# Optimization experiments

Hardware: AMD Instinct MI355X
Metric: run time of the kernel (lower is better)

The kernel has to match this reference:

```python
import jax, jax.numpy as jnp
import numpy as np

B, C, D, W, H = 8, 256, 24, 24, 24
COUT = 256
EMBED = 128
HEADS = 8
WORD = 64
POOL = 3  # forward hardcodes adaptive_avg_pool3d(x, 3)


def setup_inputs() -> dict:
    key = jax.random.key(0)
    ks = jax.random.split(key, 12)
    s = lambda n: 1.0 / np.sqrt(n)
    return {
        "x": jax.random.normal(ks[0], (B, C, D, W, H), dtype=jnp.float32),
        "qk_w": jax.random.normal(ks[1], (2 * EMBED, POOL ** 3), dtype=jnp.float32) * s(POOL ** 3),
        "qk_b": jax.random.normal(ks[2], (2 * EMBED,), dtype=jnp.float32) * 0.02,
        "wq_w": jax.random.normal(ks[3], (HEADS * WORD, EMBED), dtype=jnp.float32) * s(EMBED),
        "wq_b": jax.random.normal(ks[4], (HEADS * WORD,), dtype=jnp.float32) * 0.02,
        "wk_w": jax.random.normal(ks[5], (HEADS * WORD, EMBED), dtype=jnp.float32) * s(EMBED),
        "wk_b": jax.random.normal(ks[6], (HEADS * WORD,), dtype=jnp.float32) * 0.02,
        "fch_w": jax.random.normal(ks[7], (1, HEADS), dtype=jnp.float32) * s(HEADS),
        "fch_b": jax.random.normal(ks[8], (1,), dtype=jnp.float32) * 0.02,
        "conv_w": jax.random.normal(ks[9], (COUT, C), dtype=jnp.float32) * s(C),
        "conv_b": jax.random.normal(ks[10], (COUT,), dtype=jnp.float32) * 0.02,
    }


def reference(x, qk_w, qk_b, wq_w, wq_b, wk_w, wk_b, fch_w, fch_b, conv_w, conv_b):
    b, c, d, w, h = x.shape
    # adaptive_avg_pool3d to 3x3x3 (exact: dims divisible by 3) -> [b, c, 27]
    xmean = x.reshape(b, c, POOL, d // POOL, POOL, w // POOL, POOL, h // POOL)
    xmean = xmean.mean(axis=(3, 5, 7)).reshape(b, c, POOL ** 3)
    # qk projection -> split into q, k of [b, c, embed]
    qk = xmean @ qk_w.T + qk_b                      # [b, c, 2*embed]
    qk = qk.reshape(b, c, 2, EMBED)
    q, k = qk[:, :, 0], qk[:, :, 1]
    # head projections -> [b, heads, c, word]
    q = (q @ wq_w.T + wq_b).reshape(b, c, HEADS, WORD).transpose(0, 2, 1, 3)
    k = (k @ wk_w.T + wk_b).reshape(b, c, HEADS, WORD).transpose(0, 2, 1, 3)
    # channel attention: scores over channels [b, heads, c, c]
    scores = jnp.einsum("bhcw,bhkw->bhck", q / jnp.sqrt(jnp.float32(WORD)), k)
    attn = jax.nn.softmax(scores, axis=-1)          # dropout is identity in eval
    # v is the raw spatial map [b, c, d*w*h]; broadcast over heads
    v = x.reshape(b, c, d * w * h)
    y = jnp.einsum("bhck,bkn->bhcn", attn, v)       # [b, heads, c, dwh]
    # fch: Linear(heads, 1) combining heads
    y = jnp.einsum("bhcn,h->bcn", y, fch_w[0]) + fch_b[0]
    y = y.reshape(b, c, d, w, h)
    attn_out = jnp.einsum("bhck,h->bck", attn, fch_w[0]) + fch_b[0]  # [b, c, c]
    # 1x1x1 conv residual
    out = jnp.einsum("bcxyz,oc->boxyz", y + x, conv_w) + conv_b[None, :, None, None, None]
    return (out, attn_out)
```

## Files before the change

kernel.cpp:

```cpp
#include <hip/hip_runtime.h>
#include <cstdint>
#include <cstddef>

#define B_    8
#define C_    256
#define DWH   13824
#define P3    27
#define COUT_ 256

#define OFF_XMEAN 0
#define OFF_WQT   55296
#define OFF_WKT   69120
#define OFF_BQ    82944
#define OFF_BK    83456
#define OFF_BETA  83968
#define OFF_G     84224
#define OFF_U     90272
#define OFF_V     90488
#define OFF_D     90704
#define OFF_ZT    90712
#define OFF_A     549464
#define OFF_MHI   1073752
#define OFF_MLO   1335896

typedef __attribute__((ext_vector_type(8))) short bf16x8;
typedef __attribute__((ext_vector_type(4))) float f32x4;

__device__ __forceinline__ void split_bf16(float v, unsigned short& h, unsigned short& l) {
    unsigned u  = __float_as_uint(v);
    unsigned hu = u & 0xFFFF0000u;
    float r = v - __uint_as_float(hu);
    h = (unsigned short)(u >> 16);
    l = (unsigned short)(__float_as_uint(r) >> 16);
}

__global__ __launch_bounds__(256) void k_pool(const float* __restrict__ x,
                                              float* __restrict__ xmean) {
    int bc = blockIdx.x;
    __shared__ float p0[576], p1[576], p2[576];
    const float* xb = x + (size_t)bc * DWH;
    for (int t = threadIdx.x; t < 576; t += 256) {
        int g  = t >> 6;
        int s  = t & 63;
        int pd = g / 3, pw = g % 3;
        int d  = pd * 8 + (s >> 3);
        int w  = pw * 8 + (s & 7);
        const float4* r = (const float4*)(xb + ((size_t)d * 24 + w) * 24);
        float4 f0 = r[0], f1 = r[1], f2 = r[2], f3 = r[3], f4v = r[4], f5 = r[5];
        p0[t] = f0.x + f0.y + f0.z + f0.w + f1.x + f1.y + f1.z + f1.w;
        p1[t] = f2.x + f2.y + f2.z + f2.w + f3.x + f3.y + f3.z + f3.w;
        p2[t] = f4v.x + f4v.y + f4v.z + f4v.w + f5.x + f5.y + f5.z + f5.w;
    }
    __syncthreads();
    int tid = threadIdx.x;
    if (tid < 27) {
        int pd = tid / 9, pw = (tid / 3) % 3, ph = tid % 3;
        int g = pd * 3 + pw;
        const float* src = (ph == 0) ? p0 : (ph == 1 ? p1 : p2);
        float s = 0.f;
        #pragma unroll 8
        for (int i = 0; i < 64; ++i) s += src[g * 64 + i];
        xmean[(size_t)bc * P3 + tid] = s * (1.0f / 512.0f);
    }
}

__global__ __launch_bounds__(128) void k_combine(
    const float* __restrict__ qk_w, const float* __restrict__ qk_b,
    const float* __restrict__ wq_w, const float* __restrict__ wq_b,
    const float* __restrict__ wk_w, const float* __restrict__ wk_b,
    const float* __restrict__ fch_b, const float* __restrict__ conv_w,
    const float* __restrict__ conv_b,
    float* __restrict__ WqT, float* __restrict__ WkT,
    float* __restrict__ bq, float* __restrict__ bk, float* __restrict__ beta) {
    int t = blockIdx.x * 128 + threadIdx.x;
    if (t < 13824) {
        int j = t / 27, p = t % 27;
        float s = 0.f;
        for (int e = 0; e < 128; ++e) s += wq_w[j * 128 + e] * qk_w[e * 27 + p];
        WqT[p * 512 + j] = s;
    } else if (t < 27648) {
        int u = t - 13824, j = u / 27, p = u % 27;
        float s = 0.f;
        for (int e = 0; e < 128; ++e) s += wk_w[j * 128 + e] * qk_w[(128 + e) * 27 + p];
        WkT[p * 512 + j] = s;
    } else if (t < 28160) {
        int j = t - 27648;
        float s = wq_b[j];
        for (int e = 0; e < 128; ++e) s += wq_w[j * 128 + e] * qk_b[e];
        bq[j] = s;
    } else if (t < 28672) {
        int j = t - 28160;
        float s = wk_b[j];
        for (int e = 0; e < 128; ++e) s += wk_w[j * 128 + e] * qk_b[128 + e];
        bk[j] = s;
    } else if (t < 28928) {
        int o = t - 28672;
        float s = 0.f;
        for (int c = 0; c < 256; ++c) s += conv_w[o * 256 + c];
        beta[o] = fch_b[0] * s + conv_b[o];
    }
}

__global__ __launch_bounds__(256) void k_G(
    const float* __restrict__ WqT, const float* __restrict__ WkT,
    const float* __restrict__ bq, const float* __restrict__ bk,
    float* __restrict__ G, float* __restrict__ U,
    float* __restrict__ V, float* __restrict__ D) {
    int h = blockIdx.x;
    int base = h * 64;
    for (int idx = threadIdx.x; idx < 811; idx += 256) {
        if (idx < 756) {
            int p = idx / 28, r = idx % 28;
            float s = 0.f;
            if (r < 27)
                for (int w = 0; w < 64; ++w)
                    s += WqT[p * 512 + base + w] * WkT[r * 512 + base + w];
            G[(h * 27 + p) * 28 + r] = 0.125f * s;
        } else if (idx < 783) {
            int p = idx - 756;
            float s = 0.f;
            for (int w = 0; w < 64; ++w) s += WqT[p * 512 + base + w] * bk[base + w];
            V[h * 27 + p] = 0.125f * s;
        } else if (idx < 810) {
            int r = idx - 783;
            float s = 0.f;
            for (int w = 0; w < 64; ++w) s += WkT[r * 512 + base + w] * bq[base + w];
            U[h * 27 + r] = 0.125f * s;
        } else {
            float s = 0.f;
            for (int w = 0; w < 64; ++w) s += bq[base + w] * bk[base + w];
            D[h] = 0.125f * s;
        }
    }
}

__global__ __launch_bounds__(256) void k_z(
    const float* __restrict__ xmean, const float* __restrict__ G,
    const float* __restrict__ U, const float* __restrict__ V,
    const float* __restrict__ D, float* __restrict__ ZT) {
    int h = blockIdx.x, b = blockIdx.y;
    int k = threadIdx.x;
    __shared__ float Gs[756], Us[27], Vs[27], Ds;
    for (int idx = threadIdx.x; idx < 756; idx += 256) Gs[idx] = G[h * 756 + idx];
    if (threadIdx.x < 27) { Us[threadIdx.x] = U[h * 27 + threadIdx.x];
                            Vs[threadIdx.x] = V[h * 27 + threadIdx.x]; }
    if (threadIdx.x == 27) Ds = D[h];
    __syncthreads();
    float xm[28];
    const float* xp = xmean + ((size_t)(b * C_) + k) * P3;
    #pragma unroll
    for (int r = 0; r < 27; ++r) xm[r] = xp[r];
    xm[27] = 0.f;
    float z[28];
    #pragma unroll
    for (int p = 0; p < 27; ++p) {
        float acc = Vs[p];
        #pragma unroll
        for (int r4 = 0; r4 < 7; ++r4) {
            float4 g = *(const float4*)&Gs[p * 28 + r4 * 4];
            acc += g.x * xm[r4 * 4] + g.y * xm[r4 * 4 + 1]
                 + g.z * xm[r4 * 4 + 2] + g.w * xm[r4 * 4 + 3];
        }
        z[p] = acc;
    }
    {
        float e = Ds;
        #pragma unroll
        for (int r = 0; r < 27; ++r) e += Us[r] * xm[r];
        z[27] = e;
    }
    float4* zt = (float4*)ZT;
    int bh = b * 8 + h;
    #pragma unroll
    for (int p4 = 0; p4 < 7; ++p4) {
        float4 v = {z[p4 * 4], z[p4 * 4 + 1], z[p4 * 4 + 2], z[p4 * 4 + 3]};
        zt[((size_t)(bh * 7 + p4)) * 256 + k] = v;
    }
}

__global__ __launch_bounds__(256) void k_attn(
    const float* __restrict__ xmean, const float* __restrict__ ZT,
    const float* __restrict__ fch_w, const float* __restrict__ fch_b,
    float* __restrict__ A, float* __restrict__ attn_out) {
    int b = blockIdx.y;
    int c0 = blockIdx.x * 4;
    int t = threadIdx.x;
    int lane = t & 63, wv = t >> 6;
    __shared__ float xsh[4 * 28];
    __shared__ float ss[4][256];
    __shared__ float mx[4], den[4];
    if (t < 112) {
        int i = t / 28, p = t % 28;
        xsh[t] = (p < 27) ? xmean[((size_t)(b * C_) + c0 + i) * P3 + p] : 1.0f;
    }
    __syncthreads();
    float4 xr[4][7];
    #pragma unroll
    for (int cl = 0; cl < 4; ++cl)
        #pragma unroll
        for (int p4 = 0; p4 < 7; ++p4)
            xr[cl][p4] = *(const float4*)&xsh[cl * 28 + p4 * 4];
    float areg[4] = {0.f, 0.f, 0.f, 0.f};
    const float4* zt = (const float4*)ZT;
    for (int h = 0; h < 8; ++h) {
        int bh = b * 8 + h;
        float4 zk[7];
        #pragma unroll
        for (int p4 = 0; p4 < 7; ++p4)
            zk[p4] = zt[((size_t)(bh * 7 + p4)) * 256 + t];
        #pragma unroll
        for (int cl = 0; cl < 4; ++cl) {
            float dot = 0.f;
            #pragma unroll
            for (int p4 = 0; p4 < 7; ++p4) {
                float4 xv = xr[cl][p4];
                float4 zv = zk[p4];
                dot += xv.x * zv.x + xv.y * zv.y + xv.z * zv.z + xv.w * zv.w;
            }
            ss[cl][t] = dot;
        }
        __syncthreads();
        {
            int cl = wv;
            float4 v = *(const float4*)&ss[cl][lane * 4];
            float m = fmaxf(fmaxf(v.x, v.y), fmaxf(v.z, v.w));
            for (int off = 32; off; off >>= 1) m = fmaxf(m, __shfl_xor(m, off, 64));
            float s = expf(v.x - m) + expf(v.y - m) + expf(v.z - m) + expf(v.w - m);
            for (int off = 32; off; off >>= 1) s += __shfl_xor(s, off, 64);
            if (lane == 0) { mx[cl] = m; den[cl] = s; }
        }
        __syncthreads();
        float fw = fch_w[h];
        #pragma unroll
        for (int cl = 0; cl < 4; ++cl)
            areg[cl] += expf(ss[cl][t] - mx[cl]) * (fw / den[cl]);
        __syncthreads();
    }
    float fb = fch_b[0];
    #pragma unroll
    for (int cl = 0; cl < 4; ++cl) {
        size_t idx = ((size_t)(b * C_) + c0 + cl) * C_ + t;
        A[idx] = areg[cl];
        attn_out[idx] = areg[cl] + fb;
    }
}

__global__ __launch_bounds__(256) void k_M(
    const float* __restrict__ A, const float* __restrict__ conv_w,
    unsigned short* __restrict__ Mhi, unsigned short* __restrict__ Mlo) {
    int b = blockIdx.y;
    int o0 = blockIdx.x * 8;
    int t = threadIdx.x;
    __shared__ float cw[8][256];
    #pragma unroll
    for (int r = 0; r < 8; ++r) cw[r][t] = conv_w[(o0 + r) * 256 + t];
    __syncthreads();
    float acc[8] = {0.f, 0.f, 0.f, 0.f, 0.f, 0.f, 0.f, 0.f};
    const float* Ab = A + (size_t)b * C_ * C_;
    for (int c = 0; c < 256; ++c) {
        float av = Ab[(size_t)c * 256 + t];
        #pragma unroll
        for (int r = 0; r < 8; ++r) acc[r] += cw[r][c] * av;
    }
    #pragma unroll
    for (int r = 0; r < 8; ++r) {
        float mv = acc[r] + conv_w[(o0 + r) * 256 + t];
        unsigned short h, l;
        split_bf16(mv, h, l);
        size_t idx = ((size_t)(b * C_) + o0 + r) * 256 + t;
        Mhi[idx] = h;
        Mlo[idx] = l;
    }
}

__global__ __launch_bounds__(256, 2) void k_out_mfma(
    const unsigned short* __restrict__ Mhi, const unsigned short* __restrict__ Mlo,
    const float* __restrict__ x, const float* __restrict__ beta,
    float* __restrict__ out) {
    int b  = blockIdx.y;
    int n0 = blockIdx.x * 64;
    int t  = threadIdx.x;
    int lane = t & 63, wv = t >> 6;
    int wo   = wv * 64;
    int l15  = lane & 15;
    int kseg = lane >> 4;
    int kbyte = kseg * 16;

    __shared__ __align__(16) unsigned short MsH[256 * 32];
    __shared__ __align__(16) unsigned short MsL[256 * 32];
    __shared__ __align__(16) unsigned short XsH[64 * 32];
    __shared__ __align__(16) unsigned short XsL[64 * 32];

    f32x4 acc[4][4];
    #pragma unroll
    for (int m = 0; m < 4; ++m)
        #pragma unroll
        for (int nf = 0; nf < 4; ++nf) acc[m][nf] = (f32x4){0.f, 0.f, 0.f, 0.f};

    const float* xb = x + (size_t)b * 256 * DWH;
    const unsigned short* gh = Mhi + (size_t)b * 256 * 256;
    const unsigned short* gl = Mlo + (size_t)b * 256 * 256;

    for (int k0 = 0; k0 < 256; k0 += 32) {
        if (k0) __syncthreads();
        {
            int c4   = t & 3;
            int orow = t >> 2;
            #pragma unroll
            for (int it = 0; it < 4; ++it) {
                int o = it * 64 + orow;
                size_t gidx = (size_t)o * 256 + k0 + c4 * 8;
                uint4 vh = *(const uint4*)(gh + gidx);
                uint4 vl = *(const uint4*)(gl + gidx);
                int off = o * 64 + ((c4 * 16) ^ ((o & 3) << 4));
                *(uint4*)((char*)MsH + off) = vh;
                *(uint4*)((char*)MsL + off) = vl;
            }
        }
        {
            int n     = t & 63;
            int khalf = t >> 6;
            const float* xcol = xb + (size_t)(k0 + khalf * 8) * DWH + n0 + n;
            unsigned h[8], l[8];
            #pragma unroll
            for (int j = 0; j < 8; ++j) {
                float v = xcol[(size_t)j * DWH];
                unsigned short hh, ll;
                split_bf16(v, hh, ll);
                h[j] = hh; l[j] = ll;
            }
            uint4 vh, vl;
            vh.x = h[0] | (h[1] << 16); vh.y = h[2] | (h[3] << 16);
            vh.z = h[4] | (h[5] << 16); vh.w = h[6] | (h[7] << 16);
            vl.x = l[0] | (l[1] << 16); vl.y = l[2] | (l[3] << 16);
            vl.z = l[4] | (l[5] << 16); vl.w = l[6] | (l[7] << 16);
            int off = n * 64 + ((khalf * 16) ^ ((n & 3) << 4));
            *(uint4*)((char*)XsH + off) = vh;
            *(uint4*)((char*)XsL + off) = vl;
        }
        __syncthreads();
        bf16x8 Ah[4], Al[4], Bh[4], Bl[4];
        #pragma unroll
        for (int m = 0; m < 4; ++m) {
            int o = wo + m * 16 + l15;
            int off = o * 64 + (kbyte ^ ((o & 3) << 4));
            Ah[m] = *(const bf16x8*)((const char*)MsH + off);
            Al[m] = *(const bf16x8*)((const char*)MsL + off);
        }
        #pragma unroll
        for (int nf = 0; nf < 4; ++nf) {
            int n = nf * 16 + l15;
            int off = n * 64 + (kbyte ^ ((n & 3) << 4));
            Bh[nf] = *(const bf16x8*)((const char*)XsH + off);
            Bl[nf] = *(const bf16x8*)((const char*)XsL + off);
        }
        #pragma unroll
        for (int m = 0; m < 4; ++m)
            #pragma unroll
            for (int nf = 0; nf < 4; ++nf) {
                f32x4 c = acc[m][nf];
                c = __builtin_amdgcn_mfma_f32_16x16x32_bf16(Al[m], Bh[nf], c, 0, 0, 0);
                c = __builtin_amdgcn_mfma_f32_16x16x32_bf16(Ah[m], Bl[nf], c, 0, 0, 0);
                c = __builtin_amdgcn_mfma_f32_16x16x32_bf16(Ah[m], Bh[nf], c, 0, 0, 0);
                acc[m][nf] = c;
            }
    }

    int r4 = (lane >> 4) * 4;
    #pragma unroll
    for (int m = 0; m < 4; ++m) {
        int obase = wo + m * 16 + r4;
        float bet[4];
        #pragma unroll
        for (int r = 0; r < 4; ++r) bet[r] = beta[obase + r];
        #pragma unroll
        for (int nf = 0; nf < 4; ++nf) {
            int n = n0 + nf * 16 + l15;
            #pragma unroll
            for (int r = 0; r < 4; ++r)
                out[((size_t)(b * 256 + obase + r)) * DWH + n] = acc[m][nf][r] + bet[r];
        }
    }
}

extern "C" void kernel_launch(void* const* d_in, const int* in_sizes, int n_in,
                              void* d_out, int out_size, void* d_ws, size_t ws_size,
                              hipStream_t stream) {
    const float* x      = (const float*)d_in[0];
    const float* qk_w   = (const float*)d_in[1];
    const float* qk_b   = (const float*)d_in[2];
    const float* wq_w   = (const float*)d_in[3];
    const float* wq_b   = (const float*)d_in[4];
    const float* wk_w   = (const float*)d_in[5];
    const float* wk_b   = (const float*)d_in[6];
    const float* fch_w  = (const float*)d_in[7];
    const float* fch_b  = (const float*)d_in[8];
    const float* conv_w = (const float*)d_in[9];
    const float* conv_b = (const float*)d_in[10];
    float* out = (float*)d_out;
    float* attn_out = out + (size_t)B_ * COUT_ * DWH;
    float* ws = (float*)d_ws;
    unsigned short* Mhi = (unsigned short*)(ws + OFF_MHI);
    unsigned short* Mlo = (unsigned short*)(ws + OFF_MLO);

    k_pool<<<B_ * C_, 256, 0, stream>>>(x, ws + OFF_XMEAN);
    k_combine<<<226, 128, 0, stream>>>(qk_w, qk_b, wq_w, wq_b, wk_w, wk_b,
                                       fch_b, conv_w, conv_b,
                                       ws + OFF_WQT, ws + OFF_WKT,
                                       ws + OFF_BQ, ws + OFF_BK, ws + OFF_BETA);
    k_G<<<8, 256, 0, stream>>>(ws + OFF_WQT, ws + OFF_WKT, ws + OFF_BQ, ws + OFF_BK,
                               ws + OFF_G, ws + OFF_U, ws + OFF_V, ws + OFF_D);
    k_z<<<dim3(8, B_), 256, 0, stream>>>(ws + OFF_XMEAN, ws + OFF_G, ws + OFF_U,
                                         ws + OFF_V, ws + OFF_D, ws + OFF_ZT);
    k_attn<<<dim3(64, B_), 256, 0, stream>>>(ws + OFF_XMEAN, ws + OFF_ZT, fch_w, fch_b,
                                             ws + OFF_A, attn_out);
    k_M<<<dim3(32, B_), 256, 0, stream>>>(ws + OFF_A, conv_w, Mhi, Mlo);
    k_out_mfma<<<dim3(216, B_), 256, 0, stream>>>(Mhi, Mlo, x, ws + OFF_BETA, out);
}
```

Baseline: 145.0 us.

## Fuse prep kernels, pre-pack M fragments, and cut MFMA passes on x

```diff
diff --git a/kernel.cpp b/kernel.cpp
--- a/kernel.cpp
+++ b/kernel.cpp
@@ -9,19 +9,11 @@
 #define COUT_ 256
 
 #define OFF_XMEAN 0
-#define OFF_WQT   55296
-#define OFF_WKT   69120
-#define OFF_BQ    82944
-#define OFF_BK    83456
-#define OFF_BETA  83968
-#define OFF_G     84224
-#define OFF_U     90272
-#define OFF_V     90488
-#define OFF_D     90704
-#define OFF_ZT    90712
-#define OFF_A     549464
-#define OFF_MHI   1073752
-#define OFF_MLO   1335896
+#define OFF_BETA  55296
+#define OFF_ZT    55552
+#define OFF_A     514304
+#define OFF_MPH   1038592
+#define OFF_MPL   1300736
 
 typedef __attribute__((ext_vector_type(8))) short bf16x8;
 typedef __attribute__((ext_vector_type(4))) float f32x4;
@@ -32,6 +24,13 @@
     float r = v - __uint_as_float(hu);
     h = (unsigned short)(u >> 16);
     l = (unsigned short)(__float_as_uint(r) >> 16);
+}
+
+__device__ __forceinline__ unsigned rne2(float a, float b) {
+    unsigned ua = __float_as_uint(a), ub = __float_as_uint(b);
+    unsigned ra = (ua + 0x7FFFu + ((ua >> 16) & 1u)) >> 16;
+    unsigned rb = (ub + 0x7FFFu + ((ub >> 16) & 1u)) >> 16;
+    return ra | (rb << 16);
 }
 
 __global__ __launch_bounds__(256) void k_pool(const float* __restrict__ x,
@@ -64,88 +63,63 @@
     }
 }
 
-__global__ __launch_bounds__(128) void k_combine(
+__global__ __launch_bounds__(256) void k_prep(
     const float* __restrict__ qk_w, const float* __restrict__ qk_b,
     const float* __restrict__ wq_w, const float* __restrict__ wq_b,
     const float* __restrict__ wk_w, const float* __restrict__ wk_b,
-    const float* __restrict__ fch_b, const float* __restrict__ conv_w,
-    const float* __restrict__ conv_b,
-    float* __restrict__ WqT, float* __restrict__ WkT,
-    float* __restrict__ bq, float* __restrict__ bk, float* __restrict__ beta) {
-    int t = blockIdx.x * 128 + threadIdx.x;
-    if (t < 13824) {
-        int j = t / 27, p = t % 27;
-        float s = 0.f;
-        for (int e = 0; e < 128; ++e) s += wq_w[j * 128 + e] * qk_w[e * 27 + p];
-        WqT[p * 512 + j] = s;
-    } else if (t < 27648) {
-        int u = t - 13824, j = u / 27, p = u % 27;
-        float s = 0.f;
-        for (int e = 0; e < 128; ++e) s += wk_w[j * 128 + e] * qk_w[(128 + e) * 27 + p];
-        WkT[p * 512 + j] = s;
-    } else if (t < 28160) {
-        int j = t - 27648;
-        float s = wq_b[j];
-        for (int e = 0; e < 128; ++e) s += wq_w[j * 128 + e] * qk_b[e];
-        bq[j] = s;
-    } else if (t < 28672) {
-        int j = t - 28160;
-        float s = wk_b[j];
-        for (int e = 0; e < 128; ++e) s += wk_w[j * 128 + e] * qk_b[128 + e];
-        bk[j] = s;
-    } else if (t < 28928) {
-        int o = t - 28672;
-        float s = 0.f;
-        for (int c = 0; c < 256; ++c) s += conv_w[o * 256 + c];
-        beta[o] = fch_b[0] * s + conv_b[o];
-    }
-}
-
-__global__ __launch_bounds__(256) void k_G(
-    const float* __restrict__ WqT, const float* __restrict__ WkT,
-    const float* __restrict__ bq, const float* __restrict__ bk,
-    float* __restrict__ G, float* __restrict__ U,
-    float* __restrict__ V, float* __restrict__ D) {
-    int h = blockIdx.x;
-    int base = h * 64;
-    for (int idx = threadIdx.x; idx < 811; idx += 256) {
+    const float* __restrict__ xmean, float* __restrict__ ZT) {
+    int h = blockIdx.x, b = blockIdx.y;
+    int t = threadIdx.x;
+    __shared__ float Wq[P3][64], Wk[P3][64];
+    __shared__ float bqs[64], bks[64];
+    __shared__ float Gs[756], Us[P3], Vs[P3], Ds;
+    for (int idx = t; idx < 1728; idx += 256) {
+        int p = idx >> 6, w = idx & 63;
+        int row = h * 64 + w;
+        float sq = 0.f, sk = 0.f;
+        for (int e = 0; e < 128; ++e) {
+            float wqv = wq_w[row * 128 + e];
+            float wkv = wk_w[row * 128 + e];
+            sq += wqv * qk_w[e * 27 + p];
+            sk += wkv * qk_w[(128 + e) * 27 + p];
+        }
+        Wq[p][w] = sq; Wk[p][w] = sk;
+    }
+    if (t < 64) {
+        int row = h * 64 + t;
+        float s1 = wq_b[row], s2 = wk_b[row];
+        for (int e = 0; e < 128; ++e) {
+            s1 += wq_w[row * 128 + e] * qk_b[e];
+            s2 += wk_w[row * 128 + e] * qk_b[128 + e];
+        }
+        bqs[t] = s1; bks[t] = s2;
+    }
+    __syncthreads();
+    for (int idx = t; idx < 811; idx += 256) {
         if (idx < 756) {
             int p = idx / 28, r = idx % 28;
             float s = 0.f;
             if (r < 27)
-                for (int w = 0; w < 64; ++w)
-                    s += WqT[p * 512 + base + w] * WkT[r * 512 + base + w];
-            G[(h * 27 + p) * 28 + r] = 0.125f * s;
+                for (int w = 0; w < 64; ++w) s += Wq[p][w] * Wk[r][w];
+            Gs[p * 28 + r] = 0.125f * s;
         } else if (idx < 783) {
             int p = idx - 756;
             float s = 0.f;
-            for (int w = 0; w < 64; ++w) s += WqT[p * 512 + base + w] * bk[base + w];
-            V[h * 27 + p] = 0.125f * s;
+            for (int w = 0; w < 64; ++w) s += Wq[p][w] * bks[w];
+            Vs[p] = 0.125f * s;
         } else if (idx < 810) {
             int r = idx - 783;
             float s = 0.f;
-            for (int w = 0; w < 64; ++w) s += WkT[r * 512 + base + w] * bq[base + w];
-            U[h * 27 + r] = 0.125f * s;
+            for (int w = 0; w < 64; ++w) s += Wk[r][w] * bqs[w];
+            Us[r] = 0.125f * s;
         } else {
             float s = 0.f;
-            for (int w = 0; w < 64; ++w) s += bq[base + w] * bk[base + w];
-            D[h] = 0.125f * s;
-        }
-    }
-}
-
-__global__ __launch_bounds__(256) void k_z(
-    const float* __restrict__ xmean, const float* __restrict__ G,
-    const float* __restrict__ U, const float* __restrict__ V,
-    const float* __restrict__ D, float* __restrict__ ZT) {
-    int h = blockIdx.x, b = blockIdx.y;
-    int k = threadIdx.x;
-    __shared__ float Gs[756], Us[27], Vs[27], Ds;
-    for (int idx = threadIdx.x; idx < 756; idx += 256) Gs[idx] = G[h * 756 + idx];
-    if (threadIdx.x < 27) { Us[threadIdx.x] = U[h * 27 + threadIdx.x];
-                            Vs[threadIdx.x] = V[h * 27 + threadIdx.x]; }
-    if (threadIdx.x == 27) Ds = D[h];
-    __syncthreads();
+            for (int w = 0; w < 64; ++w) s += bqs[w] * bks[w];
+            Ds = 0.125f * s;
+        }
+    }
+    __syncthreads();
+    int k = t;
     float xm[28];
     const float* xp = xmean + ((size_t)(b * C_) + k) * P3;
     #pragma unroll
@@ -247,7 +221,9 @@
 
 __global__ __launch_bounds__(256) void k_M(
     const float* __restrict__ A, const float* __restrict__ conv_w,
-    unsigned short* __restrict__ Mhi, unsigned short* __restrict__ Mlo) {
+    const float* __restrict__ fch_b, const float* __restrict__ conv_b,
+    unsigned short* __restrict__ MpH, unsigned short* __restrict__ MpL,
+    float* __restrict__ beta) {
     int b = blockIdx.y;
     int o0 = blockIdx.x * 8;
     int t = threadIdx.x;
@@ -262,34 +238,38 @@
         #pragma unroll
         for (int r = 0; r < 8; ++r) acc[r] += cw[r][c] * av;
     }
+    if (b == 0 && t < 8) {
+        float s = 0.f;
+        for (int c = 0; c < 256; ++c) s += cw[t][c];
+        beta[o0 + t] = fch_b[0] * s + conv_b[o0 + t];
+    }
+    int ks = t >> 5, e = t & 7;
+    int lanehi = ((t >> 3) & 3) << 4;
+    size_t base = ((size_t)(b * 8 + ks) * 16 + (o0 >> 4)) * 64;
+    int osub = (o0 & 8);
     #pragma unroll
     for (int r = 0; r < 8; ++r) {
-        float mv = acc[r] + conv_w[(o0 + r) * 256 + t];
+        float mv = acc[r] + cw[r][t];
         unsigned short h, l;
         split_bf16(mv, h, l);
-        size_t idx = ((size_t)(b * C_) + o0 + r) * 256 + t;
-        Mhi[idx] = h;
-        Mlo[idx] = l;
-    }
-}
-
-__global__ __launch_bounds__(256, 2) void k_out_mfma(
-    const unsigned short* __restrict__ Mhi, const unsigned short* __restrict__ Mlo,
+        size_t idx = (base + ((osub + r) | lanehi)) * 8 + e;
+        MpH[idx] = h;
+        MpL[idx] = l;
+    }
+}
+
+__global__ __launch_bounds__(256, 3) void k_out_mfma(
+    const bf16x8* __restrict__ MpH, const bf16x8* __restrict__ MpL,
     const float* __restrict__ x, const float* __restrict__ beta,
     float* __restrict__ out) {
     int b  = blockIdx.y;
     int n0 = blockIdx.x * 64;
     int t  = threadIdx.x;
     int lane = t & 63, wv = t >> 6;
-    int wo   = wv * 64;
     int l15  = lane & 15;
     int kseg = lane >> 4;
-    int kbyte = kseg * 16;
-
-    __shared__ __align__(16) unsigned short MsH[256 * 32];
-    __shared__ __align__(16) unsigned short MsL[256 * 32];
-    __shared__ __align__(16) unsigned short XsH[64 * 32];
-    __shared__ __align__(16) unsigned short XsL[64 * 32];
+
+    __shared__ __align__(16) unsigned short Xs[2][64 * 32];
 
     f32x4 acc[4][4];
     #pragma unroll
@@ -298,75 +278,67 @@
         for (int nf = 0; nf < 4; ++nf) acc[m][nf] = (f32x4){0.f, 0.f, 0.f, 0.f};
 
     const float* xb = x + (size_t)b * 256 * DWH;
-    const unsigned short* gh = Mhi + (size_t)b * 256 * 256;
-    const unsigned short* gl = Mlo + (size_t)b * 256 * 256;
-
-    for (int k0 = 0; k0 < 256; k0 += 32) {
-        if (k0) __syncthreads();
-        {
-            int c4   = t & 3;
-            int orow = t >> 2;
+    const bf16x8* mh = MpH + (size_t)b * 8192;
+    const bf16x8* ml = MpL + (size_t)b * 8192;
+
+    int sn = t & 63;
+    int sk = t >> 6;
+    const float* xcol0 = xb + (size_t)(sk * 8) * DWH + n0 + sn;
+    int soff = sn * 64 + ((sk * 16) ^ (((sn >> 1) & 3) << 4));
+
+    {
+        float xr[8];
+        #pragma unroll
+        for (int j = 0; j < 8; ++j) xr[j] = xcol0[(size_t)j * DWH];
+        uint4 v;
+        v.x = rne2(xr[0], xr[1]); v.y = rne2(xr[2], xr[3]);
+        v.z = rne2(xr[4], xr[5]); v.w = rne2(xr[6], xr[7]);
+        *(uint4*)((char*)Xs[0] + soff) = v;
+    }
+    __syncthreads();
+
+    for (int s = 0; s < 8; ++s) {
+        int cur = s & 1;
+        float xn[8];
+        if (s < 7) {
+            const float* xc = xcol0 + (size_t)((s + 1) * 32) * DWH;
             #pragma unroll
-            for (int it = 0; it < 4; ++it) {
-                int o = it * 64 + orow;
-                size_t gidx = (size_t)o * 256 + k0 + c4 * 8;
-                uint4 vh = *(const uint4*)(gh + gidx);
-                uint4 vl = *(const uint4*)(gl + gidx);
-                int off = o * 64 + ((c4 * 16) ^ ((o & 3) << 4));
-                *(uint4*)((char*)MsH + off) = vh;
-                *(uint4*)((char*)MsL + off) = vl;
-            }
-        }
-        {
-            int n     = t & 63;
-            int khalf = t >> 6;
-            const float* xcol = xb + (size_t)(k0 + khalf * 8) * DWH + n0 + n;
-            unsigned h[8], l[8];
-            #pragma unroll
-            for (int j = 0; j < 8; ++j) {
-                float v = xcol[(size_t)j * DWH];
-                unsigned short hh, ll;
-                split_bf16(v, hh, ll);
-                h[j] = hh; l[j] = ll;
-            }
-            uint4 vh, vl;
-            vh.x = h[0] | (h[1] << 16); vh.y = h[2] | (h[3] << 16);
-            vh.z = h[4] | (h[5] << 16); vh.w = h[6] | (h[7] << 16);
-            vl.x = l[0] | (l[1] << 16); vl.y = l[2] | (l[3] << 16);
-            vl.z = l[4] | (l[5] << 16); vl.w = l[6] | (l[7] << 16);
-            int off = n * 64 + ((khalf * 16) ^ ((n & 3) << 4));
-            *(uint4*)((char*)XsH + off) = vh;
-            *(uint4*)((char*)XsL + off) = vl;
-        }
-        __syncthreads();
-        bf16x8 Ah[4], Al[4], Bh[4], Bl[4];
+            for (int j = 0; j < 8; ++j) xn[j] = xc[(size_t)j * DWH];
+        }
+        bf16x8 Ah[4], Al[4];
         #pragma unroll
         for (int m = 0; m < 4; ++m) {
-            int o = wo + m * 16 + l15;
-            int off = o * 64 + (kbyte ^ ((o & 3) << 4));
-            Ah[m] = *(const bf16x8*)((const char*)MsH + off);
-            Al[m] = *(const bf16x8*)((const char*)MsL + off);
-        }
+            int idx = (s * 16 + wv * 4 + m) * 64 + lane;
+            Ah[m] = mh[idx];
+            Al[m] = ml[idx];
+        }
+        bf16x8 Bf[4];
         #pragma unroll
         for (int nf = 0; nf < 4; ++nf) {
             int n = nf * 16 + l15;
-            int off = n * 64 + (kbyte ^ ((n & 3) << 4));
-            Bh[nf] = *(const bf16x8*)((const char*)XsH + off);
-            Bl[nf] = *(const bf16x8*)((const char*)XsL + off);
+            int off = n * 64 + ((kseg * 16) ^ (((n >> 1) & 3) << 4));
+            Bf[nf] = *(const bf16x8*)((const char*)Xs[cur] + off);
         }
         #pragma unroll
         for (int m = 0; m < 4; ++m)
             #pragma unroll
             for (int nf = 0; nf < 4; ++nf) {
                 f32x4 c = acc[m][nf];
-                c = __builtin_amdgcn_mfma_f32_16x16x32_bf16(Al[m], Bh[nf], c, 0, 0, 0);
-                c = __builtin_amdgcn_mfma_f32_16x16x32_bf16(Ah[m], Bl[nf], c, 0, 0, 0);
-                c = __builtin_amdgcn_mfma_f32_16x16x32_bf16(Ah[m], Bh[nf], c, 0, 0, 0);
+                c = __builtin_amdgcn_mfma_f32_16x16x32_bf16(Al[m], Bf[nf], c, 0, 0, 0);
+                c = __builtin_amdgcn_mfma_f32_16x16x32_bf16(Ah[m], Bf[nf], c, 0, 0, 0);
                 acc[m][nf] = c;
             }
+        if (s < 7) {
+            uint4 v;
+            v.x = rne2(xn[0], xn[1]); v.y = rne2(xn[2], xn[3]);
+            v.z = rne2(xn[4], xn[5]); v.w = rne2(xn[6], xn[7]);
+            *(uint4*)((char*)Xs[cur ^ 1] + soff) = v;
+        }
+        __syncthreads();
     }
 
     int r4 = (lane >> 4) * 4;
+    int wo = wv * 64;
     #pragma unroll
     for (int m = 0; m < 4; ++m) {
         int obase = wo + m * 16 + r4;
@@ -400,20 +372,16 @@
     float* out = (float*)d_out;
     float* attn_out = out + (size_t)B_ * COUT_ * DWH;
     float* ws = (float*)d_ws;
-    unsigned short* Mhi = (unsigned short*)(ws + OFF_MHI);
-    unsigned short* Mlo = (unsigned short*)(ws + OFF_MLO);
+    unsigned short* MpH = (unsigned short*)(ws + OFF_MPH);
+    unsigned short* MpL = (unsigned short*)(ws + OFF_MPL);
 
     k_pool<<<B_ * C_, 256, 0, stream>>>(x, ws + OFF_XMEAN);
-    k_combine<<<226, 128, 0, stream>>>(qk_w, qk_b, wq_w, wq_b, wk_w, wk_b,
-                                       fch_b, conv_w, conv_b,
-                                       ws + OFF_WQT, ws + OFF_WKT,
-                                       ws + OFF_BQ, ws + OFF_BK, ws + OFF_BETA);
-    k_G<<<8, 256, 0, stream>>>(ws + OFF_WQT, ws + OFF_WKT, ws + OFF_BQ, ws + OFF_BK,
-                               ws + OFF_G, ws + OFF_U, ws + OFF_V, ws + OFF_D);
-    k_z<<<dim3(8, B_), 256, 0, stream>>>(ws + OFF_XMEAN, ws + OFF_G, ws + OFF_U,
-                                         ws + OFF_V, ws + OFF_D, ws + OFF_ZT);
+    k_prep<<<dim3(8, B_), 256, 0, stream>>>(qk_w, qk_b, wq_w, wq_b, wk_w, wk_b,
+                                            ws + OFF_XMEAN, ws + OFF_ZT);
     k_attn<<<dim3(64, B_), 256, 0, stream>>>(ws + OFF_XMEAN, ws + OFF_ZT, fch_w, fch_b,
                                              ws + OFF_A, attn_out);
-    k_M<<<dim3(32, B_), 256, 0, stream>>>(ws + OFF_A, conv_w, Mhi, Mlo);
-    k_out_mfma<<<dim3(216, B_), 256, 0, stream>>>(Mhi, Mlo, x, ws + OFF_BETA, out);
-}
+    k_M<<<dim3(32, B_), 256, 0, stream>>>(ws + OFF_A, conv_w, fch_b, conv_b,
+                                          MpH, MpL, ws + OFF_BETA);
+    k_out_mfma<<<dim3(216, B_), 256, 0, stream>>>((const bf16x8*)MpH, (const bf16x8*)MpL,
+                                                  x, ws + OFF_BETA, out);
+}
```

Result: slower. 179.8 us (+24.0%).
